# Kernel tuning notes

Hardware: AMD Instinct MI355X
Metric: run time of the kernel (lower is better)

## Reference

```python
import jax, jax.numpy as jnp
import numpy as np

P = 2013265921  # BabyBear prime, 15*2^27 + 1 (NTT-friendly stand-in for the 256-bit BLS12-381 field)
GEN = 31        # generator of the multiplicative group of F_P
COSET_G = 3     # coset shift generator
B, N = 8, 1 << 22


def _pow_table(base, n, p):
    """[1, base, base^2, ..., base^{n-1}] mod p via log-doubling (numpy, exact int64)."""
    t = np.ones(n, dtype=np.int64)
    cur = base % p
    k = 1
    while k < n:
        m = min(k, n - k)
        t[k:k + m] = (t[:m] * cur) % p
        cur = (cur * cur) % p
        k *= 2
    return t


def _bitrev(n):
    logn = n.bit_length() - 1
    idx = np.arange(n, dtype=np.int64)
    r = np.zeros(n, dtype=np.int64)
    for i in range(logn):
        r = (r << 1) | ((idx >> i) & 1)
    return r


def _ntt(x, tw, brev, p):
    """Iterative Cooley-Tukey DIT NTT. x: [B, N] int64 in [0, p). tw: [N/2] powers of omega."""
    b, n = x.shape
    x = x[:, brev]
    m = 2
    while m <= n:
        half = m // 2
        w = tw[:: n // m][:half]              # omega^{k * N/m}, k = 0..half-1
        x = x.reshape(b, n // m, m)
        u = x[:, :, :half]
        v = (x[:, :, half:] * w) % p          # < 2^62, safe in int64
        x = jnp.concatenate([(u + v) % p, (u - v) % p], axis=-1).reshape(b, n)
        m *= 2
    return x


def setup_inputs() -> dict:
    key = jax.random.key(0)
    inp = jax.random.randint(key, (B, N), 0, P, dtype=jnp.int64)
    omega = pow(GEN, (P - 1) // N, P)
    omega_inv = pow(omega, -1, P)
    twiddles = jnp.asarray(_pow_table(omega, N // 2, P))
    inv_twiddles = jnp.asarray(_pow_table(omega_inv, N // 2, P))
    coset_powers = jnp.asarray(_pow_table(COSET_G, N, P))
    inv_coset_powers = jnp.asarray(_pow_table(pow(COSET_G, -1, P), N, P))
    bitrev = jnp.asarray(_bitrev(N))
    return {
        "input": inp,
        "twiddles": twiddles,
        "inv_twiddles": inv_twiddles,
        "coset_powers": coset_powers,
        "inv_coset_powers": inv_coset_powers,
        "bitrev": bitrev,
        "is_intt": 0,
        "is_coset": 1,
    }


def reference(input, twiddles, inv_twiddles, coset_powers, inv_coset_powers, bitrev, is_intt, is_coset):
    n = input.shape[-1]
    if is_intt and is_coset:
        out = _ntt(input, inv_twiddles, bitrev, P)
        out = (out * pow(n, -1, P)) % P
        out = (out * inv_coset_powers) % P
    elif is_intt:
        out = _ntt(input, inv_twiddles, bitrev, P)
        out = (out * pow(n, -1, P)) % P
    elif is_coset:
        x = (input * coset_powers) % P
        out = _ntt(x, twiddles, bitrev, P)
    else:
        out = _ntt(input, twiddles, bitrev, P)
    return out
```

## Files before the change

kernel.cpp:

```cpp
#include <hip/hip_runtime.h>
#include <stdint.h>

#define P_MOD       2013265921u
#define TWO32_MOD_P 268435454u

__device__ __forceinline__ uint32_t umin32(uint32_t a, uint32_t b) { return a < b ? a : b; }

__device__ __forceinline__ uint32_t wrapmod(uint32_t z) {
    uint32_t t = z - ((uint32_t)((int32_t)z >> 31) & TWO32_MOD_P);
    return umin32(t, t - P_MOD);
}

__device__ __forceinline__ uint32_t addmod_w(uint32_t u, uint32_t t2) {
    return wrapmod(u + t2);
}

__device__ __forceinline__ uint32_t submod_w(uint32_t u, uint32_t t2) {
    uint32_t d = u - t2;
    return umin32(d, d + P_MOD);
}

__device__ __forceinline__ uint32_t mulmod_wrap(uint32_t a, uint32_t b) {
    return wrapmod(a * b);
}

__host__ __device__ constexpr uint32_t compute_pinv_neg() {
    uint32_t x = 1u;
    for (int i = 0; i < 5; ++i) x *= (2u - P_MOD * x);
    return 0u - x;
}
#define PINV_NEG (compute_pinv_neg())
constexpr uint32_t R2_MOD_P = (uint32_t)(((unsigned __int128)1 << 64) % P_MOD);

__device__ __forceinline__ uint32_t montmul(uint32_t a, uint32_t b) {
    uint32_t lo = a * b;
    uint32_t hi = __umulhi(a, b);
    uint32_t m  = lo * PINV_NEG;
    uint32_t t  = hi + __umulhi(m, P_MOD) + (lo != 0u);
    return umin32(t, t - P_MOD);
}

typedef uint32_t u32x4 __attribute__((ext_vector_type(4)));
__device__ __forceinline__ uint4 nt_load4(const uint32_t* p) {
    u32x4 v = __builtin_nontemporal_load(reinterpret_cast<const u32x4*>(p));
    return make_uint4(v.x, v.y, v.z, v.w);
}
__device__ __forceinline__ void nt_store4(uint32_t* p, uint4 x) {
    u32x4 v = {x.x, x.y, x.z, x.w};
    __builtin_nontemporal_store(v, reinterpret_cast<u32x4*>(p));
}

__global__ __launch_bounds__(256) void ntt_pack(
    const uint32_t* __restrict__ tw,
    const uint32_t* __restrict__ itw,
    const int* __restrict__ f_intt,
    uint32_t* __restrict__ ptw, int logn)
{
    int idx = blockIdx.x * 256 + threadIdx.x;
    if (idx >= 8128) return;
    const uint32_t* __restrict__ twsel = f_intt[0] ? itw : tw;
    uint32_t v = (uint32_t)idx + 64u;
    int pm1 = 31 - __clz(v);
    int j   = (int)(v - (1u << pm1));
    int pa  = pm1 + 1;
    ptw[idx] = twsel[(uint32_t)j << (logn - pa)];
}

__global__ __launch_bounds__(256) void ntt_k1(
    const uint32_t* __restrict__ in,
    const uint32_t* __restrict__ tw,
    const uint32_t* __restrict__ itw,
    const uint32_t* __restrict__ cp,
    const int* __restrict__ f_intt,
    const int* __restrict__ f_coset,
    uint32_t* __restrict__ out,
    int logn)
{
    __shared__ uint32_t sh[64 * 65];
    const int tid = threadIdx.x;
    const int w   = blockIdx.x;
    const long long base = (long long)blockIdx.y << logn;

    const int is_intt  = f_intt[0];
    const bool do_coset = (!is_intt) && (f_coset[0] != 0);
    const uint32_t* __restrict__ twsel = is_intt ? itw : tw;

    const uint32_t wrev = __brev((uint32_t)w) >> (32 - (logn - 12));

    const int s4 = tid & 15;
    const uint32_t ub = __brev((uint32_t)s4) >> 28;
    for (int it = 0; it < 4; ++it) {
        int c = (it << 4) | (tid >> 4);
        uint32_t crev = __brev((uint32_t)c) >> 26;
        long long src = ((long long)crev << (logn - 6)) |
                        ((long long)wrev << 6) | (unsigned)(s4 << 2);
        uint4 x = nt_load4(in + base + src);
        if (do_coset) {
            uint4 cv = nt_load4(cp + src);
            x.x = mulmod_wrap(x.x, cv.x);
            x.y = mulmod_wrap(x.y, cv.y);
            x.z = mulmod_wrap(x.z, cv.z);
            x.w = mulmod_wrap(x.w, cv.w);
        }
        sh[(ub     ) * 65 + c] = x.x;
        sh[(ub + 32) * 65 + c] = x.y;
        sh[(ub + 16) * 65 + c] = x.z;
        sh[(ub + 48) * 65 + c] = x.w;
    }
    __syncthreads();

    for (int pa = 1; pa <= 6; ++pa) {
        const int hs   = 1 << (pa - 1);
        const int twsh = logn - pa;
        for (int it = 0; it < 8; ++it) {
            int bf   = tid + it * 256;
            int row  = bf >> 5;
            int cb   = bf & 31;
            int j    = cb & (hs - 1);
            int cblk = cb >> (pa - 1);
            int cu   = (cblk << pa) | j;
            int cv   = cu + hs;
            uint32_t u = sh[row * 65 + cu];
            uint32_t v = sh[row * 65 + cv];
            uint32_t t2 = mulmod_wrap(v, twsel[(uint32_t)j << twsh]);
            sh[row * 65 + cu] = addmod_w(u, t2);
            sh[row * 65 + cv] = submod_w(u, t2);
        }
        __syncthreads();
    }

    for (int it = 0; it < 4; ++it) {
        int u  = (it << 4) | (tid >> 4);
        int cb = (tid & 15) << 2;
        uint4 x;
        x.x = sh[u * 65 + cb    ];
        x.y = sh[u * 65 + cb + 1];
        x.z = sh[u * 65 + cb + 2];
        x.w = sh[u * 65 + cb + 3];
        long long dst = ((long long)u << (logn - 6)) |
                        ((long long)w << 6) | (unsigned)cb;
        *(uint4*)(out + base + dst) = x;
    }
}

__global__ __launch_bounds__(512, 8) void ntt_k2(
    const uint32_t* __restrict__ tw,
    const uint32_t* __restrict__ itw,
    const int* __restrict__ f_intt,
    const uint32_t* __restrict__ ptw,
    uint32_t* __restrict__ data,
    int logn)
{
    alignas(16) __shared__ uint32_t sh[8192];
    const int tid = threadIdx.x;
    const long long base = ((long long)blockIdx.y << logn) +
                           ((long long)blockIdx.x << 13);
    const uint32_t* __restrict__ twsel = f_intt[0] ? itw : tw;

    for (int it = 0; it < 4; ++it) {
        int t4 = tid + it * 512;
        uint4 x = nt_load4(data + base + (t4 << 2));
        ((uint4*)sh)[t4] = x;
    }
    __syncthreads();

    for (int pa = 7; pa <= 13; ++pa) {
        const int hs    = 1 << (pa - 1);
        const int twsh  = logn - pa;
        const int pbase = hs - 64;
        for (int it = 0; it < 2; ++it) {
            int q  = tid + it * 512;
            int jq = q & ((hs >> 2) - 1);
            int blk= q >> (pa - 3);
            int j  = jq << 2;
            int iu = (blk << pa) | j;
            int iv = iu + hs;
            uint4 u = *(const uint4*)&sh[iu];
            uint4 v = *(const uint4*)&sh[iv];
            uint4 wv;
            if (ptw) {
                wv = *(const uint4*)&ptw[pbase + j];
            } else {
                wv.x = twsel[(uint32_t)(j    ) << twsh];
                wv.y = twsel[(uint32_t)(j + 1) << twsh];
                wv.z = twsel[(uint32_t)(j + 2) << twsh];
                wv.w = twsel[(uint32_t)(j + 3) << twsh];
            }
            uint32_t t0 = mulmod_wrap(v.x, wv.x);
            uint32_t t1 = mulmod_wrap(v.y, wv.y);
            uint32_t t2 = mulmod_wrap(v.z, wv.z);
            uint32_t t3 = mulmod_wrap(v.w, wv.w);
            uint4 ru = make_uint4(addmod_w(u.x, t0), addmod_w(u.y, t1),
                                  addmod_w(u.z, t2), addmod_w(u.w, t3));
            uint4 rv = make_uint4(submod_w(u.x, t0), submod_w(u.y, t1),
                                  submod_w(u.z, t2), submod_w(u.w, t3));
            *(uint4*)&sh[iu] = ru;
            *(uint4*)&sh[iv] = rv;
        }
        __syncthreads();
    }

    for (int it = 0; it < 4; ++it) {
        int t4 = tid + it * 512;
        ((uint4*)(data + base))[t4] = ((const uint4*)sh)[t4];
    }
}

__global__ __launch_bounds__(1024, 8) void ntt_k3(
    const uint32_t* __restrict__ tw,
    const uint32_t* __restrict__ itw,
    const uint32_t* __restrict__ icp,
    const int* __restrict__ f_intt,
    const int* __restrict__ f_coset,
    uint32_t* __restrict__ data,
    uint32_t ninv, int logn)
{
    alignas(16) __shared__ uint32_t sh[512 * 32];
    alignas(16) __shared__ uint32_t shB[9 * 32];
    __shared__ uint32_t shA[511];
    const int tid = threadIdx.x;
    const long long base = (long long)blockIdx.y << logn;
    const int lowbase = blockIdx.x * 32;

    const int is_intt  = f_intt[0];
    const int is_coset = f_coset[0];
    const uint32_t* __restrict__ twsel = is_intt ? itw : tw;

    if (tid < 511) {
        uint32_t v = (uint32_t)tid + 1u;
        int p  = 31 - __clz(v);
        int sj = (int)(v - (1u << p));
        uint32_t wa = twsel[(uint32_t)sj << (21 - p)];
        shA[tid] = montmul(wa, R2_MOD_P);
    } else if (tid >= 512 && tid < 512 + 288) {
        int k = tid - 512, p = k >> 5, lo = k & 31;
        shB[k] = twsel[(uint32_t)(lowbase + lo) << (8 - p)];
    }

    for (int it = 0; it < 4; ++it) {
        int e4  = tid + it * 1024;
        int lo4 = e4 & 7;
        int s   = e4 >> 3;
        uint4 x = nt_load4(data + base + ((long long)s << 13) + lowbase + (lo4 << 2));
        *(uint4*)&sh[(s << 5) | (lo4 << 2)] = x;
    }
    __syncthreads();

    for (int p = 0; p <= 2; ++p) {
        const int hs = 1 << p;
        for (int it = 0; it < 8; ++it) {
            int bf   = tid + it * 1024;
            int lo   = bf & 31;
            int sb   = bf >> 5;
            int sj   = sb & (hs - 1);
            int sblk = sb >> p;
            int su   = (sblk << (p + 1)) | sj;
            int sv   = su + hs;
            uint32_t u = sh[(su << 5) | lo];
            uint32_t v = sh[(sv << 5) | lo];
            uint32_t wv = montmul(shA[(hs - 1) + sj], shB[(p << 5) | lo]);
            uint32_t t2 = mulmod_wrap(v, wv);
            sh[(su << 5) | lo] = addmod_w(u, t2);
            sh[(sv << 5) | lo] = submod_w(u, t2);
        }
        __syncthreads();
    }

    for (int p = 3; p <= 8; ++p) {
        const int hs = 1 << p;
        for (int it = 0; it < 2; ++it) {
            int q    = tid + it * 1024;
            int l4   = (q & 7) << 2;
            int sb   = q >> 3;
            int sj   = sb & (hs - 1);
            int sblk = sb >> p;
            int su   = (sblk << (p + 1)) | sj;
            int sv   = su + hs;
            uint4 u = *(const uint4*)&sh[(su << 5) | l4];
            uint4 v = *(const uint4*)&sh[(sv << 5) | l4];
            uint32_t wa = shA[(hs - 1) + sj];
            uint4 wb = *(const uint4*)&shB[(p << 5) | l4];
            uint32_t t0 = mulmod_wrap(v.x, montmul(wa, wb.x));
            uint32_t t1 = mulmod_wrap(v.y, montmul(wa, wb.y));
            uint32_t t2 = mulmod_wrap(v.z, montmul(wa, wb.z));
            uint32_t t3 = mulmod_wrap(v.w, montmul(wa, wb.w));
            uint4 ru = make_uint4(addmod_w(u.x, t0), addmod_w(u.y, t1),
                                  addmod_w(u.z, t2), addmod_w(u.w, t3));
            uint4 rv = make_uint4(submod_w(u.x, t0), submod_w(u.y, t1),
                                  submod_w(u.z, t2), submod_w(u.w, t3));
            *(uint4*)&sh[(su << 5) | l4] = ru;
            *(uint4*)&sh[(sv << 5) | l4] = rv;
        }
        __syncthreads();
    }

    for (int it = 0; it < 4; ++it) {
        int e4  = tid + it * 1024;
        int lo4 = e4 & 7;
        int s   = e4 >> 3;
        uint4 val = *(const uint4*)&sh[(s << 5) | (lo4 << 2)];
        long long gi = ((long long)s << 13) + lowbase + (lo4 << 2);
        if (is_intt) {
            val.x = mulmod_wrap(val.x, ninv);
            val.y = mulmod_wrap(val.y, ninv);
            val.z = mulmod_wrap(val.z, ninv);
            val.w = mulmod_wrap(val.w, ninv);
            if (is_coset) {
                uint4 ic = *(const uint4*)(icp + gi);
                val.x = mulmod_wrap(val.x, ic.x);
                val.y = mulmod_wrap(val.y, ic.y);
                val.z = mulmod_wrap(val.z, ic.z);
                val.w = mulmod_wrap(val.w, ic.w);
            }
        }
        nt_store4(data + base + gi, val);
    }
}

extern "C" void kernel_launch(void* const* d_in, const int* in_sizes, int n_in,
                              void* d_out, int out_size, void* d_ws, size_t ws_size,
                              hipStream_t stream) {
    const uint32_t* in  = (const uint32_t*)d_in[0];
    const uint32_t* tw  = (const uint32_t*)d_in[1];
    const uint32_t* itw = (const uint32_t*)d_in[2];
    const uint32_t* cp  = (const uint32_t*)d_in[3];
    const uint32_t* icp = (const uint32_t*)d_in[4];
    const int* f_intt  = (const int*)d_in[6];
    const int* f_coset = (const int*)d_in[7];

    const int N = in_sizes[5];
    const int B = in_sizes[0] / N;
    int logn = 0; while ((1 << logn) < N) ++logn;

    const unsigned long long P = 2013265921ull;
    unsigned long long b = (unsigned long long)N % P, e = P - 2, acc = 1;
    while (e) { if (e & 1) acc = acc * b % P; b = b * b % P; e >>= 1; }
    const uint32_t ninv = (uint32_t)acc;

    uint32_t* out = (uint32_t*)d_out;

    uint32_t* ptw = (ws_size >= 8128u * 4u) ? (uint32_t*)d_ws : nullptr;
    if (ptw) ntt_pack<<<dim3(32), dim3(256), 0, stream>>>(tw, itw, f_intt, ptw, logn);

    dim3 g1(N / 4096, B);
    ntt_k1<<<g1, dim3(256), 0, stream>>>(in, tw, itw, cp, f_intt, f_coset, out, logn);

    dim3 g2(N / 8192, B);
    ntt_k2<<<g2, dim3(512), 0, stream>>>(tw, itw, f_intt, ptw, out, logn);

    dim3 g3(8192 / 32, B);
    ntt_k3<<<g3, dim3(1024), 0, stream>>>(tw, itw, icp, f_intt, f_coset, out, ninv, logn);
}
```

Measured before the change: 528.5 us.

## Fuse NTT butterfly stages into radix-4/radix-8 passes in shared memory

Rewrites the in-shared-memory butterfly loops of all three NTT kernels so each thread holds 4 or 8 elements in registers and applies two or three radix-2 stages before writing back. This cuts shared-memory round trips and barrier count per stage. k1 also caches its stage twiddles in a small shared table, and launch-bounds occupancy hints drop from 8 to 4 to leave room for the extra registers. The cost is higher register pressure and possible LDS bank conflicts from the strided per-thread access patterns.

```diff
diff --git a/kernel.cpp b/kernel.cpp
--- a/kernel.cpp
+++ b/kernel.cpp
@@ -10,18 +10,21 @@
     uint32_t t = z - ((uint32_t)((int32_t)z >> 31) & TWO32_MOD_P);
     return umin32(t, t - P_MOD);
 }
-
 __device__ __forceinline__ uint32_t addmod_w(uint32_t u, uint32_t t2) {
     return wrapmod(u + t2);
 }
-
 __device__ __forceinline__ uint32_t submod_w(uint32_t u, uint32_t t2) {
     uint32_t d = u - t2;
     return umin32(d, d + P_MOD);
 }
-
 __device__ __forceinline__ uint32_t mulmod_wrap(uint32_t a, uint32_t b) {
     return wrapmod(a * b);
+}
+__device__ __forceinline__ void bf_w(uint32_t& u, uint32_t& v, uint32_t w) {
+    uint32_t t  = mulmod_wrap(v, w);
+    uint32_t nu = addmod_w(u, t);
+    v = submod_w(u, t);
+    u = nu;
 }
 
 __host__ __device__ constexpr uint32_t compute_pinv_neg() {
@@ -66,7 +69,7 @@
     ptw[idx] = twsel[(uint32_t)j << (logn - pa)];
 }
 
-__global__ __launch_bounds__(256) void ntt_k1(
+__global__ __launch_bounds__(256, 4) void ntt_k1(
     const uint32_t* __restrict__ in,
     const uint32_t* __restrict__ tw,
     const uint32_t* __restrict__ itw,
@@ -77,6 +80,7 @@
     int logn)
 {
     __shared__ uint32_t sh[64 * 65];
+    __shared__ uint32_t shT[32];
     const int tid = threadIdx.x;
     const int w   = blockIdx.x;
     const long long base = (long long)blockIdx.y << logn;
@@ -84,6 +88,8 @@
     const int is_intt  = f_intt[0];
     const bool do_coset = (!is_intt) && (f_coset[0] != 0);
     const uint32_t* __restrict__ twsel = is_intt ? itw : tw;
+
+    if (tid < 32) shT[tid] = twsel[(uint32_t)tid << (logn - 6)];
 
     const uint32_t wrev = __brev((uint32_t)w) >> (32 - (logn - 12));
 
@@ -109,22 +115,25 @@
     }
     __syncthreads();
 
-    for (int pa = 1; pa <= 6; ++pa) {
-        const int hs   = 1 << (pa - 1);
-        const int twsh = logn - pa;
-        for (int it = 0; it < 8; ++it) {
-            int bf   = tid + it * 256;
-            int row  = bf >> 5;
-            int cb   = bf & 31;
-            int j    = cb & (hs - 1);
-            int cblk = cb >> (pa - 1);
-            int cu   = (cblk << pa) | j;
-            int cv   = cu + hs;
-            uint32_t u = sh[row * 65 + cu];
-            uint32_t v = sh[row * 65 + cv];
-            uint32_t t2 = mulmod_wrap(v, twsel[(uint32_t)j << twsh]);
-            sh[row * 65 + cu] = addmod_w(u, t2);
-            sh[row * 65 + cv] = submod_w(u, t2);
+#pragma unroll
+    for (int pa = 1; pa <= 5; pa += 2) {
+        const int hs = 1 << (pa - 1);
+        const int row = tid & 63;
+        for (int it = 0; it < 4; ++it) {
+            int q    = (tid >> 6) + (it << 2);
+            int cj   = q & (hs - 1);
+            int cblk = q >> (pa - 1);
+            int c0   = (cblk << (pa + 1)) | cj;
+            int b    = row * 65 + c0;
+            uint32_t e0 = sh[b], e1 = sh[b + hs], e2 = sh[b + 2*hs], e3 = sh[b + 3*hs];
+            uint32_t w0 = shT[cj << (6 - pa)];
+            uint32_t w1 = shT[cj << (5 - pa)];
+            uint32_t w2 = shT[(cj + hs) << (5 - pa)];
+            bf_w(e0, e1, w0);
+            bf_w(e2, e3, w0);
+            bf_w(e0, e2, w1);
+            bf_w(e1, e3, w2);
+            sh[b] = e0; sh[b + hs] = e1; sh[b + 2*hs] = e2; sh[b + 3*hs] = e3;
         }
         __syncthreads();
     }
@@ -143,7 +152,7 @@
     }
 }
 
-__global__ __launch_bounds__(512, 8) void ntt_k2(
+__global__ __launch_bounds__(512, 4) void ntt_k2(
     const uint32_t* __restrict__ tw,
     const uint32_t* __restrict__ itw,
     const int* __restrict__ f_intt,
@@ -159,43 +168,70 @@
 
     for (int it = 0; it < 4; ++it) {
         int t4 = tid + it * 512;
-        uint4 x = nt_load4(data + base + (t4 << 2));
-        ((uint4*)sh)[t4] = x;
+        ((uint4*)sh)[t4] = nt_load4(data + base + (t4 << 2));
     }
     __syncthreads();
 
-    for (int pa = 7; pa <= 13; ++pa) {
-        const int hs    = 1 << (pa - 1);
-        const int twsh  = logn - pa;
-        const int pbase = hs - 64;
+#pragma unroll
+    for (int pa = 7; pa <= 11; pa += 2) {
+        const int hs  = 1 << (pa - 1);
+        const int pb0 = hs - 64;
+        const int pb1 = 2 * hs - 64;
+        int q    = tid;
+        int jq   = q & ((hs >> 2) - 1);
+        int sblk = q >> (pa - 3);
+        int j    = jq << 2;
+        int i0   = (sblk << (pa + 1)) | j;
+        uint4 e0 = *(const uint4*)&sh[i0];
+        uint4 e1 = *(const uint4*)&sh[i0 + hs];
+        uint4 e2 = *(const uint4*)&sh[i0 + 2*hs];
+        uint4 e3 = *(const uint4*)&sh[i0 + 3*hs];
+        uint4 w0, w1a, w1b;
+        if (ptw) {
+            w0  = *(const uint4*)&ptw[pb0 + j];
+            w1a = *(const uint4*)&ptw[pb1 + j];
+            w1b = *(const uint4*)&ptw[pb1 + hs + j];
+        } else {
+            const int t0s = logn - pa, t1s = logn - pa - 1;
+            w0  = make_uint4(twsel[(uint32_t)(j)<<t0s], twsel[(uint32_t)(j+1)<<t0s],
+                             twsel[(uint32_t)(j+2)<<t0s], twsel[(uint32_t)(j+3)<<t0s]);
+            w1a = make_uint4(twsel[(uint32_t)(j)<<t1s], twsel[(uint32_t)(j+1)<<t1s],
+                             twsel[(uint32_t)(j+2)<<t1s], twsel[(uint32_t)(j+3)<<t1s]);
+            w1b = make_uint4(twsel[(uint32_t)(j+hs)<<t1s], twsel[(uint32_t)(j+hs+1)<<t1s],
+                             twsel[(uint32_t)(j+hs+2)<<t1s], twsel[(uint32_t)(j+hs+3)<<t1s]);
+        }
+        bf_w(e0.x, e1.x, w0.x); bf_w(e0.y, e1.y, w0.y);
+        bf_w(e0.z, e1.z, w0.z); bf_w(e0.w, e1.w, w0.w);
+        bf_w(e2.x, e3.x, w0.x); bf_w(e2.y, e3.y, w0.y);
+        bf_w(e2.z, e3.z, w0.z); bf_w(e2.w, e3.w, w0.w);
+        bf_w(e0.x, e2.x, w1a.x); bf_w(e0.y, e2.y, w1a.y);
+        bf_w(e0.z, e2.z, w1a.z); bf_w(e0.w, e2.w, w1a.w);
+        bf_w(e1.x, e3.x, w1b.x); bf_w(e1.y, e3.y, w1b.y);
+        bf_w(e1.z, e3.z, w1b.z); bf_w(e1.w, e3.w, w1b.w);
+        *(uint4*)&sh[i0         ] = e0;
+        *(uint4*)&sh[i0 +   hs  ] = e1;
+        *(uint4*)&sh[i0 + 2*hs  ] = e2;
+        *(uint4*)&sh[i0 + 3*hs  ] = e3;
+        __syncthreads();
+    }
+
+    {
+        const int hs = 4096, pb = hs - 64;
         for (int it = 0; it < 2; ++it) {
-            int q  = tid + it * 512;
-            int jq = q & ((hs >> 2) - 1);
-            int blk= q >> (pa - 3);
-            int j  = jq << 2;
-            int iu = (blk << pa) | j;
-            int iv = iu + hs;
-            uint4 u = *(const uint4*)&sh[iu];
-            uint4 v = *(const uint4*)&sh[iv];
+            int j  = (tid + it * 512) << 2;
+            uint4 u = *(const uint4*)&sh[j];
+            uint4 v = *(const uint4*)&sh[j + hs];
             uint4 wv;
-            if (ptw) {
-                wv = *(const uint4*)&ptw[pbase + j];
-            } else {
-                wv.x = twsel[(uint32_t)(j    ) << twsh];
-                wv.y = twsel[(uint32_t)(j + 1) << twsh];
-                wv.z = twsel[(uint32_t)(j + 2) << twsh];
-                wv.w = twsel[(uint32_t)(j + 3) << twsh];
+            if (ptw) wv = *(const uint4*)&ptw[pb + j];
+            else {
+                const int ts = logn - 13;
+                wv = make_uint4(twsel[(uint32_t)(j)<<ts], twsel[(uint32_t)(j+1)<<ts],
+                                twsel[(uint32_t)(j+2)<<ts], twsel[(uint32_t)(j+3)<<ts]);
             }
-            uint32_t t0 = mulmod_wrap(v.x, wv.x);
-            uint32_t t1 = mulmod_wrap(v.y, wv.y);
-            uint32_t t2 = mulmod_wrap(v.z, wv.z);
-            uint32_t t3 = mulmod_wrap(v.w, wv.w);
-            uint4 ru = make_uint4(addmod_w(u.x, t0), addmod_w(u.y, t1),
-                                  addmod_w(u.z, t2), addmod_w(u.w, t3));
-            uint4 rv = make_uint4(submod_w(u.x, t0), submod_w(u.y, t1),
-                                  submod_w(u.z, t2), submod_w(u.w, t3));
-            *(uint4*)&sh[iu] = ru;
-            *(uint4*)&sh[iv] = rv;
+            bf_w(u.x, v.x, wv.x); bf_w(u.y, v.y, wv.y);
+            bf_w(u.z, v.z, wv.z); bf_w(u.w, v.w, wv.w);
+            *(uint4*)&sh[j] = u;
+            *(uint4*)&sh[j + hs] = v;
         }
         __syncthreads();
     }
@@ -206,7 +242,7 @@
     }
 }
 
-__global__ __launch_bounds__(1024, 8) void ntt_k3(
+__global__ __launch_bounds__(1024, 4) void ntt_k3(
     const uint32_t* __restrict__ tw,
     const uint32_t* __restrict__ itw,
     const uint32_t* __restrict__ icp,
@@ -230,8 +266,7 @@
         uint32_t v = (uint32_t)tid + 1u;
         int p  = 31 - __clz(v);
         int sj = (int)(v - (1u << p));
-        uint32_t wa = twsel[(uint32_t)sj << (21 - p)];
-        shA[tid] = montmul(wa, R2_MOD_P);
+        shA[tid] = montmul(twsel[(uint32_t)sj << (21 - p)], R2_MOD_P);
     } else if (tid >= 512 && tid < 512 + 288) {
         int k = tid - 512, p = k >> 5, lo = k & 31;
         shB[k] = twsel[(uint32_t)(lowbase + lo) << (8 - p)];
@@ -246,50 +281,42 @@
     }
     __syncthreads();
 
-    for (int p = 0; p <= 2; ++p) {
-        const int hs = 1 << p;
-        for (int it = 0; it < 8; ++it) {
-            int bf   = tid + it * 1024;
-            int lo   = bf & 31;
-            int sb   = bf >> 5;
-            int sj   = sb & (hs - 1);
-            int sblk = sb >> p;
-            int su   = (sblk << (p + 1)) | sj;
-            int sv   = su + hs;
-            uint32_t u = sh[(su << 5) | lo];
-            uint32_t v = sh[(sv << 5) | lo];
-            uint32_t wv = montmul(shA[(hs - 1) + sj], shB[(p << 5) | lo]);
-            uint32_t t2 = mulmod_wrap(v, wv);
-            sh[(su << 5) | lo] = addmod_w(u, t2);
-            sh[(sv << 5) | lo] = submod_w(u, t2);
-        }
-        __syncthreads();
-    }
-
-    for (int p = 3; p <= 8; ++p) {
+#pragma unroll
+    for (int p = 0; p <= 6; p += 3) {
         const int hs = 1 << p;
         for (int it = 0; it < 2; ++it) {
-            int q    = tid + it * 1024;
-            int l4   = (q & 7) << 2;
-            int sb   = q >> 3;
-            int sj   = sb & (hs - 1);
-            int sblk = sb >> p;
-            int su   = (sblk << (p + 1)) | sj;
-            int sv   = su + hs;
-            uint4 u = *(const uint4*)&sh[(su << 5) | l4];
-            uint4 v = *(const uint4*)&sh[(sv << 5) | l4];
-            uint32_t wa = shA[(hs - 1) + sj];
-            uint4 wb = *(const uint4*)&shB[(p << 5) | l4];
-            uint32_t t0 = mulmod_wrap(v.x, montmul(wa, wb.x));
-            uint32_t t1 = mulmod_wrap(v.y, montmul(wa, wb.y));
-            uint32_t t2 = mulmod_wrap(v.z, montmul(wa, wb.z));
-            uint32_t t3 = mulmod_wrap(v.w, montmul(wa, wb.w));
-            uint4 ru = make_uint4(addmod_w(u.x, t0), addmod_w(u.y, t1),
-                                  addmod_w(u.z, t2), addmod_w(u.w, t3));
-            uint4 rv = make_uint4(submod_w(u.x, t0), submod_w(u.y, t1),
-                                  submod_w(u.z, t2), submod_w(u.w, t3));
-            *(uint4*)&sh[(su << 5) | l4] = ru;
-            *(uint4*)&sh[(sv << 5) | l4] = rv;
+            int wi = tid + it * 1024;
+            int lo = wi & 31;
+            int sq = wi >> 5;
+            int sj = sq & (hs - 1);
+            int sblk = sq >> p;
+            int s0 = (sblk << (p + 3)) | sj;
+            int b  = (s0 << 5) | lo;
+            const int st = hs << 5;
+            uint32_t e0 = sh[b        ], e1 = sh[b +   st],
+                     e2 = sh[b + 2*st], e3 = sh[b + 3*st],
+                     e4 = sh[b + 4*st], e5 = sh[b + 5*st],
+                     e6 = sh[b + 6*st], e7 = sh[b + 7*st];
+            uint32_t b0 = shB[((p    ) << 5) | lo];
+            uint32_t b1 = shB[((p + 1) << 5) | lo];
+            uint32_t b2 = shB[((p + 2) << 5) | lo];
+            uint32_t tw0  = montmul(shA[(    hs - 1) + sj         ], b0);
+            uint32_t tw1a = montmul(shA[(2 * hs - 1) + sj         ], b1);
+            uint32_t tw1b = montmul(shA[(2 * hs - 1) + sj +     hs], b1);
+            uint32_t tw2a = montmul(shA[(4 * hs - 1) + sj         ], b2);
+            uint32_t tw2b = montmul(shA[(4 * hs - 1) + sj +     hs], b2);
+            uint32_t tw2c = montmul(shA[(4 * hs - 1) + sj + 2 * hs], b2);
+            uint32_t tw2d = montmul(shA[(4 * hs - 1) + sj + 3 * hs], b2);
+            bf_w(e0, e1, tw0); bf_w(e2, e3, tw0);
+            bf_w(e4, e5, tw0); bf_w(e6, e7, tw0);
+            bf_w(e0, e2, tw1a); bf_w(e1, e3, tw1b);
+            bf_w(e4, e6, tw1a); bf_w(e5, e7, tw1b);
+            bf_w(e0, e4, tw2a); bf_w(e1, e5, tw2b);
+            bf_w(e2, e6, tw2c); bf_w(e3, e7, tw2d);
+            sh[b        ] = e0; sh[b +   st] = e1;
+            sh[b + 2*st] = e2; sh[b + 3*st] = e3;
+            sh[b + 4*st] = e4; sh[b + 5*st] = e5;
+            sh[b + 6*st] = e6; sh[b + 7*st] = e7;
         }
         __syncthreads();
     }
```

New measurement: 472.0 us. 1.12x faster.
